# Kernel optimization log

Hardware: AMD Instinct MI355X
Metric: run time of the kernel (lower is better)

Reference implementation:

```python
import jax, jax.numpy as jnp
import numpy as np

THRESHOLD = 15.0
INIT_RATIO = 0.5
WINDOW_T = 100
C1 = INIT_RATIO * THRESHOLD            # 7.5, initial membrane potential
C2 = 1.0 / THRESHOLD                   # 1/15
C3 = (1.0 - INIT_RATIO) / WINDOW_T     # 0.005


def snn_layer(spikes, mem, hat_spikes, W, b):
    """One SNNLinear layer in training mode.
    spikes: [T,B,in], mem: [B,out], hat_spikes: [B,in], W: [out,in], b: [out].
    Returns (ss [T,B,out], mem_final [B,out], hat_s [B,out]).
    """
    T = spikes.shape[0]
    # delta_us = fc(spikes): [T,B,out]
    delta_us = jnp.einsum('tbi,oi->tbo', spikes, W) + b

    def step(carry, du):
        m, sum_u = carry
        m = m + du
        s = (m > THRESHOLD).astype(m.dtype)
        m = jnp.clip(m, 0.0, THRESHOLD)
        sum_u = sum_u + m
        m = m - m * s  # reset to 0 where spiked
        return (m, sum_u), s

    (mem_f, sum_u), ss = jax.lax.scan(step, (mem, jnp.zeros_like(mem)), delta_us)
    # In torch this loop runs under no_grad
    ss = jax.lax.stop_gradient(ss)
    mem_f = jax.lax.stop_gradient(mem_f)
    hat_s_fwd = jnp.mean(ss, axis=0)
    hat_u_fwd = jax.lax.stop_gradient(sum_u) / T

    # delta_u = fc(hat_spikes): grad path
    delta_u = hat_spikes @ W.T + b
    # ForwardFirstBackwardSecond: forward value hat_u_fwd, gradient flows to delta_u
    hat_u = hat_u_fwd + (delta_u - jax.lax.stop_gradient(delta_u))
    g = jnp.maximum(hat_u * C2, C3)
    hat_s = hat_s_fwd + (g - jax.lax.stop_gradient(g))
    return ss, mem_f, hat_s


def setup_inputs() -> dict:
    key = jax.random.key(0)
    ks = jax.random.split(key, 8)
    T, B = 50, 256
    shapes = [1024, 2048, 2048, 1024]
    spikes = jax.random.bernoulli(ks[0], 0.1, (T, B, shapes[0])).astype(jnp.float32)
    hat_spk = jax.random.uniform(ks[1], (B, shapes[0]), jnp.float32) * 0.2
    mem0 = jnp.full((B, shapes[1]), C1, jnp.float32)
    mem1 = jnp.full((B, shapes[2]), C1, jnp.float32)
    mem2 = jnp.full((B, shapes[3]), C1, jnp.float32)
    W0 = jax.random.normal(ks[2], (shapes[1], shapes[0]), jnp.float32)
    b0 = jax.random.normal(ks[3], (shapes[1],), jnp.float32)
    W1 = jax.random.normal(ks[4], (shapes[2], shapes[1]), jnp.float32)
    b1 = jax.random.normal(ks[5], (shapes[2],), jnp.float32)
    W2 = jax.random.normal(ks[6], (shapes[3], shapes[2]), jnp.float32)
    b2 = jax.random.normal(ks[7], (shapes[3],), jnp.float32)
    return {"spikes": spikes, "hat_spk": hat_spk, "mem0": mem0, "mem1": mem1,
            "mem2": mem2, "W0": W0, "b0": b0, "W1": W1, "b1": b1, "W2": W2, "b2": b2}


def reference(spikes, hat_spk, mem0, mem1, mem2, W0, b0, W1, b1, W2, b2):
    s, _, h = snn_layer(spikes, mem0, hat_spk, W0, b0)
    s, _, h = snn_layer(s, mem1, h, W1, b1)
    s, _, h = snn_layer(s, mem2, h, W2, b2)
    return s, h
```

## Files before the change

### kernel.cpp

```cpp
#include <hip/hip_runtime.h>
#include <cstdint>
#include <cstddef>

#define T_STEPS 50
#define BATCH   256
#define TC      10

__global__ __launch_bounds__(256)
void pack_spikes_k(const float* __restrict__ A, uint32_t* __restrict__ P) {
    const int i    = (int)blockIdx.x * 256 + (int)threadIdx.x;
    const int lane = (int)threadIdx.x & 63;
    const unsigned long long m = __ballot(A[i] != 0.0f);
    if ((lane & 31) == 0)
        P[i >> 5] = (uint32_t)((lane & 32) ? (m >> 32) : m);
}


template<int K, int O>
__global__ __launch_bounds__(256)
void gemm_k(const uint32_t* __restrict__ Ain,
            const float* __restrict__ W,
            const float* __restrict__ bias,
            float* __restrict__ DU)
{
    constexpr int NW = K / 32;
    __shared__ float Wsm[32][256];

    const int tid = (int)threadIdx.x;
    const int o_l = tid & 63;
    const int wid = tid >> 6;
    const int o0  = (int)blockIdx.x * 256;
    const int oq  = o0 + 4 * o_l;
    const int b_u = __builtin_amdgcn_readfirstlane((int)blockIdx.y * 4 + wid);
    const int tc0 = (int)blockIdx.z * TC;
    const uint32_t* __restrict__ Ab = Ain + (size_t)b_u * NW;

    const float4 bb4 = *(const float4*)(bias + oq);

    float pre[TC][4], cur[TC][4];
#pragma unroll
    for (int tt = 0; tt < TC; ++tt)
#pragma unroll
        for (int c = 0; c < 4; ++c) { pre[tt][c] = 0.0f; cur[tt][c] = 0.0f; }

    float4 pf[8];
#pragma unroll
    for (int r = 0; r < 8; ++r) {
        const int i = tid + r * 256;
        pf[r] = *(const float4*)(W + (size_t)(o0 + (i >> 3)) * K + (i & 7) * 4);
    }

    for (int wt = 0; wt < NW; ++wt) {
#pragma unroll
        for (int r = 0; r < 8; ++r) {
            const int i    = tid + r * 256;
            const int orow = i >> 3;
            const int q    = i & 7;
            const int pc   = (((orow >> 2) ^ q) << 2) | (orow & 3);
            Wsm[4 * q + 0][pc] = pf[r].x;
            Wsm[4 * q + 1][pc] = pf[r].y;
            Wsm[4 * q + 2][pc] = pf[r].z;
            Wsm[4 * q + 3][pc] = pf[r].w;
        }
        uint32_t M[TC];
#pragma unroll
        for (int tt = 0; tt < TC; ++tt)
            M[tt] = __builtin_amdgcn_readfirstlane(
                        Ab[(size_t)(tc0 + tt) * (BATCH * NW) + wt]);
        __syncthreads();

        if (wt + 1 < NW) {
#pragma unroll
            for (int r = 0; r < 8; ++r) {
                const int i = tid + r * 256;
                pf[r] = *(const float4*)(W + (size_t)(o0 + (i >> 3)) * K
                                           + (wt + 1) * 32 + (i & 7) * 4);
            }
        }

#pragma unroll 8
        for (int kk = 0; kk < 32; ++kk) {
            const float4 wv = *(const float4*)&Wsm[kk][(o_l ^ ((kk >> 2) & 7)) << 2];
#pragma unroll
            for (int tt = 0; tt < TC; ++tt) {
                const uint32_t fb = ((M[tt] >> kk) & 1u) ? 0x3f800000u : 0u;
                const float f = __builtin_bit_cast(float, fb);
                cur[tt][0] = __builtin_fmaf(f, wv.x, cur[tt][0]);
                cur[tt][1] = __builtin_fmaf(f, wv.y, cur[tt][1]);
                cur[tt][2] = __builtin_fmaf(f, wv.z, cur[tt][2]);
                cur[tt][3] = __builtin_fmaf(f, wv.w, cur[tt][3]);
            }
        }
        __syncthreads();

        if (((wt + 1) & 15) == 0) {
#pragma unroll
            for (int tt = 0; tt < TC; ++tt)
#pragma unroll
                for (int c = 0; c < 4; ++c) {
                    pre[tt][c] = pre[tt][c] + cur[tt][c];
                    cur[tt][c] = 0.0f;
                }
        }
    }

#pragma unroll
    for (int tt = 0; tt < TC; ++tt) {
        const int t = tc0 + tt;
        float4 du;
        du.x = (pre[tt][0] + cur[tt][0]) + bb4.x;
        du.y = (pre[tt][1] + cur[tt][1]) + bb4.y;
        du.z = (pre[tt][2] + cur[tt][2]) + bb4.z;
        du.w = (pre[tt][3] + cur[tt][3]) + bb4.w;
        *(float4*)(DU + (size_t)t * (BATCH * O) + (size_t)b_u * O + oq) = du;
    }
}

template<int O, bool LAST>
__global__ __launch_bounds__(256)
void scan_k(const float* __restrict__ DU,
            const float* __restrict__ mem,
            uint32_t* __restrict__ Pout,
            float* __restrict__ SSout,
            float* __restrict__ Hout)
{
    constexpr int NWO = O / 32;
    __shared__ unsigned char pk[4][64];

    const int tid = (int)threadIdx.x;
    const int o_l = tid & 63;
    const int wid = tid >> 6;
    const int b   = (int)blockIdx.y;
    const int o0  = (int)blockIdx.x * 1024 + wid * 256;
    const int oq  = o0 + 4 * o_l;

    float4 m4 = *(const float4*)(mem + (size_t)b * O + oq);
    int c0 = 0, c1 = 0, c2 = 0, c3 = 0;

    float4 du = *(const float4*)(DU + (size_t)b * O + oq);

    for (int t = 0; t < T_STEPS; ++t) {
        float4 dun;
        if (t + 1 < T_STEPS)
            dun = *(const float4*)(DU + (size_t)(t + 1) * (BATCH * O) + (size_t)b * O + oq);
        m4.x += du.x; m4.y += du.y; m4.z += du.z; m4.w += du.w;
        const bool s0 = m4.x > 15.0f, s1 = m4.y > 15.0f,
                   s2 = m4.z > 15.0f, s3 = m4.w > 15.0f;
        m4.x = fminf(fmaxf(m4.x, 0.0f), 15.0f);
        m4.y = fminf(fmaxf(m4.y, 0.0f), 15.0f);
        m4.z = fminf(fmaxf(m4.z, 0.0f), 15.0f);
        m4.w = fminf(fmaxf(m4.w, 0.0f), 15.0f);
        if (s0) { m4.x = 0.0f; ++c0; }
        if (s1) { m4.y = 0.0f; ++c1; }
        if (s2) { m4.z = 0.0f; ++c2; }
        if (s3) { m4.w = 0.0f; ++c3; }

        if (LAST) {
            *(float4*)(SSout + (size_t)t * (BATCH * O) + (size_t)b * O + oq) =
                make_float4(s0 ? 1.0f : 0.0f, s1 ? 1.0f : 0.0f,
                            s2 ? 1.0f : 0.0f, s3 ? 1.0f : 0.0f);
        } else {
            pk[wid][o_l] = (unsigned char)((s0 ? 1 : 0) | (s1 ? 2 : 0) |
                                           (s2 ? 4 : 0) | (s3 ? 8 : 0));
            __syncthreads();
            if (o_l < 8) {
                const uint2 d = *(const uint2*)&pk[wid][o_l * 8];
                uint32_t x = d.x & 0x0F0F0F0Fu;
                x = (x | (x >> 4)) & 0x00FF00FFu;
                x = (x | (x >> 8)) & 0x0000FFFFu;
                uint32_t y = d.y & 0x0F0F0F0Fu;
                y = (y | (y >> 4)) & 0x00FF00FFu;
                y = (y | (y >> 8)) & 0x0000FFFFu;
                Pout[(size_t)t * (BATCH * NWO) + (size_t)b * NWO + (o0 >> 5) + o_l]
                    = x | (y << 16);
            }
            __syncthreads();
        }
        du = dun;
    }
    if (LAST) {
        *(float4*)(Hout + (size_t)b * O + oq) =
            make_float4((float)c0 / 50.0f, (float)c1 / 50.0f,
                        (float)c2 / 50.0f, (float)c3 / 50.0f);
    }
}

template<int K, int O, bool LAST>
__global__ __launch_bounds__(256)
void snn_k(const uint32_t* __restrict__ Ain,
           const float* __restrict__ W,
           const float* __restrict__ bias,
           const float* __restrict__ mem,
           uint32_t* __restrict__ Pout,
           float* __restrict__ SSout,
           float* __restrict__ Hout)
{
    constexpr int NW  = K / 32;
    constexpr int NWO = O / 32;
    __shared__ float Wsm[32][256];
    __shared__ unsigned char pk[4][64];

    const int tid = (int)threadIdx.x;
    const int o_l = tid & 63;
    const int wid = tid >> 6;
    const int o0  = (int)blockIdx.x * 256;
    const int oq  = o0 + 4 * o_l;
    const int b_u = __builtin_amdgcn_readfirstlane((int)blockIdx.y * 4 + wid);
    const uint32_t* __restrict__ Ab = Ain + (size_t)b_u * NW;

    float4 m4 = *(const float4*)(mem + (size_t)b_u * O + oq);
    const float4 bb4 = *(const float4*)(bias + oq);
    int c0 = 0, c1 = 0, c2 = 0, c3 = 0;

    for (int tc0 = 0; tc0 < T_STEPS; tc0 += TC) {
        float pre[TC][4], cur[TC][4];
#pragma unroll
        for (int tt = 0; tt < TC; ++tt)
#pragma unroll
            for (int c = 0; c < 4; ++c) { pre[tt][c] = 0.0f; cur[tt][c] = 0.0f; }

        for (int wt = 0; wt < NW; ++wt) {
#pragma unroll
            for (int r = 0; r < 8; ++r) {
                const int i    = tid + r * 256;
                const int orow = i >> 3;
                const int q    = i & 7;
                const float4 v = *(const float4*)(W + (size_t)(o0 + orow) * K + wt * 32 + q * 4);
                const int pc   = (((orow >> 2) ^ q) << 2) | (orow & 3);
                Wsm[4 * q + 0][pc] = v.x;
                Wsm[4 * q + 1][pc] = v.y;
                Wsm[4 * q + 2][pc] = v.z;
                Wsm[4 * q + 3][pc] = v.w;
            }
            uint32_t M[TC];
#pragma unroll
            for (int tt = 0; tt < TC; ++tt)
                M[tt] = Ab[(size_t)(tc0 + tt) * (BATCH * NW) + wt];
            __syncthreads();

#pragma unroll 8
            for (int kk = 0; kk < 32; ++kk) {
                const float4 wv = *(const float4*)&Wsm[kk][(o_l ^ ((kk >> 2) & 7)) << 2];
#pragma unroll
                for (int tt = 0; tt < TC; ++tt) {
                    const float f = __builtin_bit_cast(float, ((M[tt] >> kk) & 1u) * 0x3f800000u);
                    cur[tt][0] = __builtin_fmaf(f, wv.x, cur[tt][0]);
                    cur[tt][1] = __builtin_fmaf(f, wv.y, cur[tt][1]);
                    cur[tt][2] = __builtin_fmaf(f, wv.z, cur[tt][2]);
                    cur[tt][3] = __builtin_fmaf(f, wv.w, cur[tt][3]);
                }
            }
            __syncthreads();

            if (((wt + 1) & 15) == 0) {
#pragma unroll
                for (int tt = 0; tt < TC; ++tt)
#pragma unroll
                    for (int c = 0; c < 4; ++c) {
                        pre[tt][c] = pre[tt][c] + cur[tt][c];
                        cur[tt][c] = 0.0f;
                    }
            }
        }

#pragma unroll
        for (int tt = 0; tt < TC; ++tt) {
            const int t = tc0 + tt;
            const float du0 = (pre[tt][0] + cur[tt][0]) + bb4.x;
            const float du1 = (pre[tt][1] + cur[tt][1]) + bb4.y;
            const float du2 = (pre[tt][2] + cur[tt][2]) + bb4.z;
            const float du3 = (pre[tt][3] + cur[tt][3]) + bb4.w;
            m4.x += du0; m4.y += du1; m4.z += du2; m4.w += du3;
            const bool s0 = m4.x > 15.0f, s1 = m4.y > 15.0f,
                       s2 = m4.z > 15.0f, s3 = m4.w > 15.0f;
            m4.x = fminf(fmaxf(m4.x, 0.0f), 15.0f);
            m4.y = fminf(fmaxf(m4.y, 0.0f), 15.0f);
            m4.z = fminf(fmaxf(m4.z, 0.0f), 15.0f);
            m4.w = fminf(fmaxf(m4.w, 0.0f), 15.0f);
            if (s0) { m4.x = 0.0f; ++c0; }
            if (s1) { m4.y = 0.0f; ++c1; }
            if (s2) { m4.z = 0.0f; ++c2; }
            if (s3) { m4.w = 0.0f; ++c3; }

            if (LAST) {
                *(float4*)(SSout + (size_t)t * (BATCH * O) + (size_t)b_u * O + oq) =
                    make_float4(s0 ? 1.0f : 0.0f, s1 ? 1.0f : 0.0f,
                                s2 ? 1.0f : 0.0f, s3 ? 1.0f : 0.0f);
            } else {
                pk[wid][o_l] = (unsigned char)((s0 ? 1 : 0) | (s1 ? 2 : 0) |
                                               (s2 ? 4 : 0) | (s3 ? 8 : 0));
                __syncthreads();
                if (o_l < 8) {
                    const uint2 d = *(const uint2*)&pk[wid][o_l * 8];
                    uint32_t x = d.x & 0x0F0F0F0Fu;
                    x = (x | (x >> 4)) & 0x00FF00FFu;
                    x = (x | (x >> 8)) & 0x0000FFFFu;
                    uint32_t y = d.y & 0x0F0F0F0Fu;
                    y = (y | (y >> 4)) & 0x00FF00FFu;
                    y = (y | (y >> 8)) & 0x0000FFFFu;
                    Pout[(size_t)t * (BATCH * NWO) + (size_t)b_u * NWO + (o0 >> 5) + o_l]
                        = x | (y << 16);
                }
                __syncthreads();
            }
        }
    }
    if (LAST) {
        *(float4*)(Hout + (size_t)b_u * O + oq) =
            make_float4((float)c0 / 50.0f, (float)c1 / 50.0f,
                        (float)c2 / 50.0f, (float)c3 / 50.0f);
    }
}

extern "C" void kernel_launch(void* const* d_in, const int* in_sizes, int n_in,
                              void* d_out, int out_size, void* d_ws, size_t ws_size,
                              hipStream_t stream) {
    (void)out_size;

    const float *spikes = nullptr, *mem0 = nullptr, *mem1 = nullptr, *mem2 = nullptr;
    const float *W0 = nullptr, *b0 = nullptr, *W1 = nullptr, *b1 = nullptr;
    const float *W2 = nullptr, *b2 = nullptr;
    int n2048 = 0, nW02 = 0, nMem = 0, n262k = 0;
    for (int i = 0; i < n_in; ++i) {
        const float* p = (const float*)d_in[i];
        switch (in_sizes[i]) {
            case 13107200: spikes = p; break;
            case 4194304:  W1 = p; break;
            case 1024:     b2 = p; break;
            case 2097152:  if (nW02++ == 0) W0 = p; else W2 = p; break;
            case 2048:     if (n2048++ == 0) b0 = p; else b1 = p; break;
            case 524288:   if (nMem++ == 0) mem0 = p; else mem1 = p; break;
            case 262144:   if (n262k++ == 0) ; else mem2 = p; break;
            default: break;
        }
    }
    if (!spikes || !W0 || !W1 || !W2 || !b0 || !b1 || !b2 || !mem0 || !mem1 || !mem2) {
        spikes = (const float*)d_in[0];
        mem0 = (const float*)d_in[2]; mem1 = (const float*)d_in[3];
        mem2 = (const float*)d_in[4];
        W0 = (const float*)d_in[5]; b0 = (const float*)d_in[6];
        W1 = (const float*)d_in[7]; b1 = (const float*)d_in[8];
        W2 = (const float*)d_in[9]; b2 = (const float*)d_in[10];
    }

    uint32_t* P0 = (uint32_t*)d_ws;
    uint32_t* P1 = (uint32_t*)((char*)d_ws + (2u << 20));
    uint32_t* P2 = (uint32_t*)((char*)d_ws + (6u << 20));
    float*    DU = (float*)((char*)d_ws + (16u << 20));

    float* out_s = (float*)d_out;
    float* out_h = out_s + (size_t)T_STEPS * BATCH * 1024;

    const int n_sp = T_STEPS * BATCH * 1024;
    pack_spikes_k<<<n_sp / 256, 256, 0, stream>>>(spikes, P0);

    const size_t need = (size_t)(16u << 20)
                      + (size_t)T_STEPS * BATCH * 2048 * sizeof(float);

    if (ws_size >= need) {
        gemm_k<1024, 2048><<<dim3(8, 64, 5), dim3(256), 0, stream>>>(P0, W0, b0, DU);
        scan_k<2048, false><<<dim3(2, BATCH), dim3(256), 0, stream>>>(
            DU, mem0, P1, nullptr, nullptr);
        gemm_k<2048, 2048><<<dim3(8, 64, 5), dim3(256), 0, stream>>>(P1, W1, b1, DU);
        scan_k<2048, false><<<dim3(2, BATCH), dim3(256), 0, stream>>>(
            DU, mem1, P2, nullptr, nullptr);
        gemm_k<2048, 1024><<<dim3(4, 64, 5), dim3(256), 0, stream>>>(P2, W2, b2, DU);
        scan_k<1024, true><<<dim3(1, BATCH), dim3(256), 0, stream>>>(
            DU, mem2, nullptr, out_s, out_h);
    } else {
        snn_k<1024, 2048, false><<<dim3(8, 64), dim3(256), 0, stream>>>(
            P0, W0, b0, mem0, P1, nullptr, nullptr);
        snn_k<2048, 2048, false><<<dim3(8, 64), dim3(256), 0, stream>>>(
            P1, W1, b1, mem1, P2, nullptr, nullptr);
        snn_k<2048, 1024, true><<<dim3(4, 64), dim3(256), 0, stream>>>(
            P2, W2, b2, mem2, nullptr, out_s, out_h);
    }
}
```

Baseline: 3.048 ms.

## Double-buffer weight tiles in LDS and prefetch spike masks one step ahead

The GEMM kernel now keeps two LDS weight buffers. The next tile is written into the alternate buffer after the compute loop, so only one barrier per K-step is needed instead of two. Spike-mask words for the next step are also prefetched into registers alongside the weight prefetch. This is meant to cut barrier stalls and hide load latency, at the cost of doubling LDS use to 64 KB per block (which may lower occupancy) and adding extra registers.

```diff
diff --git a/kernel.cpp b/kernel.cpp
--- a/kernel.cpp
+++ b/kernel.cpp
@@ -24,7 +24,7 @@
             float* __restrict__ DU)
 {
     constexpr int NW = K / 32;
-    __shared__ float Wsm[32][256];
+    __shared__ float Wsm[2][32][256];
 
     const int tid = (int)threadIdx.x;
     const int o_l = tid & 63;
@@ -43,47 +43,49 @@
 #pragma unroll
         for (int c = 0; c < 4; ++c) { pre[tt][c] = 0.0f; cur[tt][c] = 0.0f; }
 
+    const int s_i    = tid;
+    const int s_orow0 = s_i >> 3;
+    const int s_q    = s_i & 7;
+
     float4 pf[8];
 #pragma unroll
+    for (int r = 0; r < 8; ++r)
+        pf[r] = *(const float4*)(W + (size_t)(o0 + s_orow0 + r * 32) * K + s_q * 4);
+    uint32_t Mc[TC], Mn[TC];
+#pragma unroll
+    for (int tt = 0; tt < TC; ++tt)
+        Mc[tt] = __builtin_amdgcn_readfirstlane(
+                     Ab[(size_t)(tc0 + tt) * (BATCH * NW) + 0]);
+#pragma unroll
     for (int r = 0; r < 8; ++r) {
-        const int i = tid + r * 256;
-        pf[r] = *(const float4*)(W + (size_t)(o0 + (i >> 3)) * K + (i & 7) * 4);
-    }
+        const int orow = s_orow0 + r * 32;
+        const int pc   = (((orow >> 2) ^ s_q) << 2) | (orow & 3);
+        Wsm[0][4 * s_q + 0][pc] = pf[r].x;
+        Wsm[0][4 * s_q + 1][pc] = pf[r].y;
+        Wsm[0][4 * s_q + 2][pc] = pf[r].z;
+        Wsm[0][4 * s_q + 3][pc] = pf[r].w;
+    }
+    __syncthreads();
 
     for (int wt = 0; wt < NW; ++wt) {
-#pragma unroll
-        for (int r = 0; r < 8; ++r) {
-            const int i    = tid + r * 256;
-            const int orow = i >> 3;
-            const int q    = i & 7;
-            const int pc   = (((orow >> 2) ^ q) << 2) | (orow & 3);
-            Wsm[4 * q + 0][pc] = pf[r].x;
-            Wsm[4 * q + 1][pc] = pf[r].y;
-            Wsm[4 * q + 2][pc] = pf[r].z;
-            Wsm[4 * q + 3][pc] = pf[r].w;
-        }
-        uint32_t M[TC];
-#pragma unroll
-        for (int tt = 0; tt < TC; ++tt)
-            M[tt] = __builtin_amdgcn_readfirstlane(
-                        Ab[(size_t)(tc0 + tt) * (BATCH * NW) + wt]);
-        __syncthreads();
-
+        const int cb = wt & 1;
         if (wt + 1 < NW) {
 #pragma unroll
-            for (int r = 0; r < 8; ++r) {
-                const int i = tid + r * 256;
-                pf[r] = *(const float4*)(W + (size_t)(o0 + (i >> 3)) * K
-                                           + (wt + 1) * 32 + (i & 7) * 4);
-            }
+            for (int r = 0; r < 8; ++r)
+                pf[r] = *(const float4*)(W + (size_t)(o0 + s_orow0 + r * 32) * K
+                                           + (wt + 1) * 32 + s_q * 4);
+#pragma unroll
+            for (int tt = 0; tt < TC; ++tt)
+                Mn[tt] = __builtin_amdgcn_readfirstlane(
+                             Ab[(size_t)(tc0 + tt) * (BATCH * NW) + (wt + 1)]);
         }
 
 #pragma unroll 8
         for (int kk = 0; kk < 32; ++kk) {
-            const float4 wv = *(const float4*)&Wsm[kk][(o_l ^ ((kk >> 2) & 7)) << 2];
+            const float4 wv = *(const float4*)&Wsm[cb][kk][(o_l ^ ((kk >> 2) & 7)) << 2];
 #pragma unroll
             for (int tt = 0; tt < TC; ++tt) {
-                const uint32_t fb = ((M[tt] >> kk) & 1u) ? 0x3f800000u : 0u;
+                const uint32_t fb = ((Mc[tt] >> kk) & 1u) ? 0x3f800000u : 0u;
                 const float f = __builtin_bit_cast(float, fb);
                 cur[tt][0] = __builtin_fmaf(f, wv.x, cur[tt][0]);
                 cur[tt][1] = __builtin_fmaf(f, wv.y, cur[tt][1]);
@@ -91,7 +93,23 @@
                 cur[tt][3] = __builtin_fmaf(f, wv.w, cur[tt][3]);
             }
         }
+
+        if (wt + 1 < NW) {
+#pragma unroll
+            for (int r = 0; r < 8; ++r) {
+                const int orow = s_orow0 + r * 32;
+                const int pc   = (((orow >> 2) ^ s_q) << 2) | (orow & 3);
+                Wsm[cb ^ 1][4 * s_q + 0][pc] = pf[r].x;
+                Wsm[cb ^ 1][4 * s_q + 1][pc] = pf[r].y;
+                Wsm[cb ^ 1][4 * s_q + 2][pc] = pf[r].z;
+                Wsm[cb ^ 1][4 * s_q + 3][pc] = pf[r].w;
+            }
+        }
         __syncthreads();
+
+#pragma unroll
+        for (int tt = 0; tt < TC; ++tt)
+            Mc[tt] = Mn[tt];
 
         if (((wt + 1) & 15) == 0) {
 #pragma unroll
```

After: 3.426 ms. 12.4% more time.
